# Kernel optimization log

Hardware: AMD Instinct MI355X
Metric: run time of the kernel (lower is better)

## Reference

```python
import jax, jax.numpy as jnp
import numpy as np

D_MODEL = 1024
D_ATTN = 256


def setup_inputs() -> dict:
    key = jax.random.key(0)
    kx, kq, kk, kv = jax.random.split(key, 4)
    B, T = 4, 2048
    s = 1.0 / np.sqrt(D_MODEL)
    return {
        "x": jax.random.normal(kx, (B, T, D_MODEL), dtype=jnp.float32),
        "W_q": jax.random.normal(kq, (D_MODEL, D_ATTN), dtype=jnp.float32) * s,
        "W_k": jax.random.normal(kk, (D_MODEL, D_ATTN), dtype=jnp.float32) * s,
        "W_v": jax.random.normal(kv, (D_MODEL, D_MODEL), dtype=jnp.float32) * s,
    }


def reference(x, W_q, W_k, W_v):
    # x: [B, T, D]; single-head causal self-attention
    B, T, D = x.shape
    scale = jnp.sqrt(jnp.asarray(W_q.shape[-1], dtype=x.dtype))
    Q = jnp.einsum('btd,da->bta', x, W_q)  # [B,T,d_attn]
    K = jnp.einsum('btd,da->bta', x, W_k)  # [B,T,d_attn]
    V = jnp.einsum('btd,de->bte', x, W_v)  # [B,T,d_model]
    scores = jnp.einsum('bqa,bka->bqk', Q, K) / scale  # [B,T,T]
    causal = jnp.tril(jnp.ones((T, T), dtype=bool))
    scores = jnp.where(causal[None], scores, -jnp.inf)
    attn_weights = jax.nn.softmax(scores, axis=-1)
    attn_output = jnp.einsum('bqk,bke->bqe', attn_weights, V)  # [B,T,d_model]
    return (attn_output, attn_weights)
```

## Files before the change

kernel.cpp:

```cpp
#include <hip/hip_runtime.h>


typedef short bf16x8 __attribute__((ext_vector_type(8)));
typedef float f32x4  __attribute__((ext_vector_type(4)));
typedef unsigned int  u32x4 __attribute__((ext_vector_type(4)));
typedef unsigned short u16x4 __attribute__((ext_vector_type(4)));

static __device__ __forceinline__ unsigned short f2bf(float f) {
    union { float f; unsigned int u; } v; v.f = f;
    unsigned int u = v.u;
    return (unsigned short)((u + 0x7FFFu + ((u >> 16) & 1u)) >> 16);
}
static __device__ __forceinline__ float bf2f(unsigned short h) {
    union { unsigned int u; float f; } v; v.u = ((unsigned int)h) << 16; return v.f;
}

#define GLL(g, l) __builtin_amdgcn_global_load_lds( \
    (const __attribute__((address_space(1))) void*)(g), \
    (__attribute__((address_space(3))) void*)(l), 16, 0, 0)

#define BAR() __builtin_amdgcn_s_barrier()
#define VM8() asm volatile("s_waitcnt vmcnt(8)" ::: "memory")
#define VM0() asm volatile("s_waitcnt vmcnt(0)" ::: "memory")


#define STAGE1(AB, LDA, BB, LDB, t, p) { \
    const unsigned short* Ap_ = (AB) + (size_t)(t) * 64; \
    const unsigned short* Bp_ = (BB) + (size_t)(t) * 64; \
    _Pragma("unroll") \
    for (int i_ = 0; i_ < 4; ++i_) { \
        GLL(Ap_ + (size_t)32 * i_ * (LDA), &As[p][srow + 32 * i_][scol]); \
        GLL(Bp_ + (size_t)32 * i_ * (LDB), &Bs[p][srow + 32 * i_][scol]); \
    } }

#define PIPE_MFMA(AB, LDA, BB, LDB, NT) { \
    STAGE1(AB, LDA, BB, LDB, 0, 0); \
    STAGE1(AB, LDA, BB, LDB, 1, 1); \
    for (int t = 0; t < (NT); ++t) { \
        int p = t & 1; \
        if (t + 1 < (NT)) VM8(); else VM0(); \
        BAR(); \
        _Pragma("unroll") \
        for (int ks = 0; ks < 64; ks += 32) { \
            int fo = ks ? (sw0 ^ 32) : sw0; \
            bf16x8 af[4], bfr[4]; \
            _Pragma("unroll") \
            for (int i = 0; i < 4; ++i) af[i]  = *(const bf16x8*)(&As[p][wr + 16 * i + fr][fo]); \
            _Pragma("unroll") \
            for (int j = 0; j < 4; ++j) bfr[j] = *(const bf16x8*)(&Bs[p][wc + 16 * j + fr][fo]); \
            _Pragma("unroll") \
            for (int i = 0; i < 4; ++i) \
            _Pragma("unroll") \
                for (int j = 0; j < 4; ++j) \
                    acc[i][j] = __builtin_amdgcn_mfma_f32_16x16x32_bf16(af[i], bfr[j], acc[i][j], 0, 0, 0); \
        } \
        BAR(); \
        if (t + 2 < (NT)) STAGE1(AB, LDA, BB, LDB, t + 2, p); \
    } }

#define TILE_IDS() \
    int tid = threadIdx.x; \
    int lane = tid & 63, wave = tid >> 6; \
    int wr = (wave >> 1) * 64, wc = (wave & 1) * 64; \
    int fr = lane & 15; \
    int srow = tid >> 3, scol = (tid & 7) * 8; \
    int scolg = (((tid & 7) ^ (srow & 7)) * 8); \
    int sw0 = (((lane >> 4) ^ (fr & 7)) * 8)


__global__ __launch_bounds__(256) void prep(
    const float* __restrict__ x, const float* __restrict__ Wq,
    const float* __restrict__ Wk, const float* __restrict__ Wv,
    unsigned short* __restrict__ x_bf, unsigned short* __restrict__ Wqk_t,
    unsigned short* __restrict__ Wv_t)
{
    int bid = blockIdx.x, tid = threadIdx.x;
    if (bid < 8192) {
        int i = bid * 256 + tid;
        f32x4 v = ((const f32x4*)x)[i];
        u16x4 o;
        o[0] = f2bf(v[0]); o[1] = f2bf(v[1]); o[2] = f2bf(v[2]); o[3] = f2bf(v[3]);
        ((u16x4*)x_bf)[i] = o;
        return;
    }
    const float* W; unsigned short* Wt; int N, lb; float scale;
    if (bid < 8448)      { W = Wq; Wt = Wqk_t;              N = 256;  lb = bid - 8192; scale = 1.f / 16.f; }
    else if (bid < 8704) { W = Wk; Wt = Wqk_t + 256 * 1024; N = 256;  lb = bid - 8448; scale = 1.f; }
    else                 { W = Wv; Wt = Wv_t;               N = 1024; lb = bid - 8704; scale = 1.f; }
    int nb = N >> 5;
    int n0 = (lb % nb) * 32, k0 = (lb / nb) * 32;
    int tx = tid & 31, ty = tid >> 5;
    __shared__ float tile[32][33];
#pragma unroll
    for (int r = 0; r < 4; ++r)
        tile[ty + 8 * r][tx] = W[(size_t)(k0 + ty + 8 * r) * N + n0 + tx];
    __syncthreads();
#pragma unroll
    for (int r = 0; r < 4; ++r)
        Wt[(size_t)(n0 + ty + 8 * r) * 1024 + k0 + tx] = f2bf(tile[tx][ty + 8 * r] * scale);
}


__global__ __launch_bounds__(256) void gemm_qkvt(
    const unsigned short* __restrict__ x_bf,
    const unsigned short* __restrict__ Wqk_t,
    const unsigned short* __restrict__ Wv_t,
    unsigned short* __restrict__ QK_bf,
    unsigned short* __restrict__ Vt_bf)
{
    int bid = blockIdx.x;
    const unsigned short *A, *B; unsigned short* C; int ldc, m0, n0;
    if (bid < 512) {
        A = Wv_t; B = x_bf; C = Vt_bf; ldc = 8192;
        m0 = (bid >> 6) * 128; n0 = (bid & 63) * 128;
    } else {
        int b2 = bid - 512;
        A = x_bf; B = Wqk_t; C = QK_bf; ldc = 512;
        m0 = (b2 >> 2) * 128; n0 = (b2 & 3) * 128;
    }
    __shared__ __align__(16) unsigned short As[2][128][64];
    __shared__ __align__(16) unsigned short Bs[2][128][64];
    TILE_IDS();
    f32x4 acc[4][4] = {};
    const unsigned short* Ab = A + (size_t)(m0 + srow) * 1024 + scolg;
    const unsigned short* Bb = B + (size_t)(n0 + srow) * 1024 + scolg;
    PIPE_MFMA(Ab, 1024, Bb, 1024, 16);
#pragma unroll
    for (int i = 0; i < 4; ++i)
#pragma unroll
        for (int j = 0; j < 4; ++j)
#pragma unroll
            for (int r = 0; r < 4; ++r) {
                int row = m0 + wr + 16 * i + (lane >> 4) * 4 + r;
                int col = n0 + wc + 16 * j + fr;
                C[(size_t)row * ldc + col] = f2bf(acc[i][j][r]);
            }
}


__global__ __launch_bounds__(256) void scores_e(
    const unsigned short* __restrict__ QK, unsigned short* __restrict__ Ebf,
    float* __restrict__ partials)
{
    int lin = blockIdx.x;
    int swz = (lin & 7) * 68 + (lin >> 3);
    int b = swz / 136, t = swz - b * 136;
    int y = (int)floorf((sqrtf(8.f * (float)t + 1.f) - 1.f) * 0.5f);
    if ((y + 1) * (y + 2) / 2 <= t) ++y;
    if (y * (y + 1) / 2 > t) --y;
    int x = t - y * (y + 1) / 2;
    int m0 = y * 128, n0 = x * 128;

    const unsigned short* A  = QK + (size_t)b * 2048 * 512;
    const unsigned short* Bt = A + 256;
    unsigned short* Eb = Ebf + (size_t)b * 2048 * 2048;

    __shared__ __align__(16) unsigned short As[2][128][64];
    __shared__ __align__(16) unsigned short Bs[2][128][64];
    __shared__ float rowsum2[2][128];
    TILE_IDS();
    f32x4 acc[4][4] = {};
    const unsigned short* Ab = A  + (size_t)(m0 + srow) * 512 + scolg;
    const unsigned short* Bb = Bt + (size_t)(n0 + srow) * 512 + scolg;
    PIPE_MFMA(Ab, 512, Bb, 512, 4);

#pragma unroll
    for (int i = 0; i < 4; ++i)
#pragma unroll
        for (int r = 0; r < 4; ++r) {
            int q = m0 + wr + 16 * i + (lane >> 4) * 4 + r;
            float s = 0.f;
#pragma unroll
            for (int j = 0; j < 4; ++j) {
                int k = n0 + wc + 16 * j + fr;
                float e = (k <= q) ? __expf(acc[i][j][r]) : 0.f;
                Eb[(size_t)q * 2048 + k] = f2bf(e);
                s += e;
            }
            s += __shfl_xor(s, 1, 64); s += __shfl_xor(s, 2, 64);
            s += __shfl_xor(s, 4, 64); s += __shfl_xor(s, 8, 64);
            if (fr == 0) rowsum2[wave & 1][wr + 16 * i + (lane >> 4) * 4 + r] = s;
        }
    __syncthreads();
    if (tid < 128)
        partials[((size_t)b * 2048 + m0 + tid) * 16 + x] =
            rowsum2[0][tid] + rowsum2[1][tid];
}


__global__ __launch_bounds__(256) void pv_fin(
    const unsigned short* __restrict__ E, const unsigned short* __restrict__ Vt,
    const float* __restrict__ partials, float* __restrict__ O,
    float* __restrict__ W)
{
    int bid = blockIdx.x;
    __shared__ __align__(16) unsigned short As[2][128][64];
    __shared__ __align__(16) unsigned short Bs[2][128][64];
    __shared__ float invsh[128];

    if (bid < 512) {
        int j   = bid & 7;
        int idx = bid >> 3;
        int x   = idx & 7;
        int h   = idx >> 3;
        int b   = h >> 1;
        int y   = (h & 1) ? j : 15 - j;

        int m0 = y * 128, n0 = x * 128;
        const unsigned short* Pb = E + (size_t)b * 2048 * 2048;
        const unsigned short* Bt = Vt + (size_t)b * 2048;
        float* Ob = O + (size_t)b * 2048 * 1024;
        int nt = (y + 1) * 2;

        TILE_IDS();
        f32x4 acc[4][4] = {};

        if (tid < 128) {
            const float* pp = partials + ((size_t)b * 2048 + m0 + tid) * 16;
            float s = 0.f;
            for (int i = 0; i <= y; ++i) s += pp[i];
            invsh[tid] = 1.f / s;
        }

        const unsigned short* Ab = Pb + (size_t)(m0 + srow) * 2048 + scolg;
        const unsigned short* Bb = Bt + (size_t)(n0 + srow) * 8192 + scolg;
        PIPE_MFMA(Ab, 2048, Bb, 8192, nt);
#pragma unroll
        for (int i = 0; i < 4; ++i)
#pragma unroll
            for (int r = 0; r < 4; ++r) {
                int rloc = wr + 16 * i + (lane >> 4) * 4 + r;
                float iv = invsh[rloc];
#pragma unroll
                for (int jj = 0; jj < 4; ++jj)
                    Ob[(size_t)(m0 + rloc) * 1024 + n0 + wc + 16 * jj + fr] = acc[i][jj][r] * iv;
            }
        return;
    }

    int tid = threadIdx.x;
    int wave = tid >> 6, lane = tid & 63;
    int r = (bid - 512) * 4 + wave;
    int q = r & 2047;
    float p = (lane < 16 && lane <= (q >> 7)) ? partials[(size_t)r * 16 + lane] : 0.f;
    p += __shfl_xor(p, 1, 64); p += __shfl_xor(p, 2, 64);
    p += __shfl_xor(p, 4, 64); p += __shfl_xor(p, 8, 64);
    float iv = 1.f / __shfl(p, 0, 64);
    const unsigned short* er = E + (size_t)r * 2048;
    float* wrow = W + (size_t)r * 2048;
#pragma unroll
    for (int cc = 0; cc < 4; ++cc) {
        int c0 = lane * 8 + cc * 512;
        f32x4 o0 = {}, o1 = {};
        if (c0 <= q) {
            bf16x8 e = *(const bf16x8*)(er + c0);
#pragma unroll
            for (int j = 0; j < 4; ++j) {
                o0[j] = bf2f((unsigned short)e[j]) * iv;
                o1[j] = bf2f((unsigned short)e[j + 4]) * iv;
            }
        }
        *((f32x4*)(wrow + c0)) = o0;
        *((f32x4*)(wrow + c0) + 1) = o1;
    }
}


extern "C" void kernel_launch(void* const* d_in, const int* in_sizes, int n_in,
                              void* d_out, int out_size, void* d_ws, size_t ws_size,
                              hipStream_t stream) {
    (void)in_sizes; (void)n_in; (void)out_size; (void)ws_size;
    const float* x  = (const float*)d_in[0];
    const float* Wq = (const float*)d_in[1];
    const float* Wk = (const float*)d_in[2];
    const float* Wv = (const float*)d_in[3];
    const int B = 4, T = 2048, D = 1024;
    const int M = B * T;

    char* ws = (char*)d_ws;
    size_t off = 0;
    auto alloc = [&](size_t bytes) {
        void* p = ws + off; off += (bytes + 255) & ~(size_t)255; return p;
    };
    unsigned short* x_bf  = (unsigned short*)alloc((size_t)M * D * 2);
    unsigned short* Wqk_t = (unsigned short*)alloc((size_t)512 * D * 2);
    unsigned short* Wv_t  = (unsigned short*)alloc((size_t)D * D * 2);
    unsigned short* QK_bf = (unsigned short*)alloc((size_t)M * 512 * 2);
    unsigned short* Vt_bf = (unsigned short*)alloc((size_t)D * M * 2);
    unsigned short* E_bf  = (unsigned short*)alloc((size_t)M * T * 2);
    float*          parts = (float*)alloc((size_t)M * 16 * 4);

    float* outO = (float*)d_out;
    float* outW = (float*)d_out + (size_t)M * D;

    prep<<<dim3(8192 + 256 + 256 + 1024), 256, 0, stream>>>(
        x, Wq, Wk, Wv, x_bf, Wqk_t, Wv_t);

    gemm_qkvt<<<dim3(768), 256, 0, stream>>>(x_bf, Wqk_t, Wv_t, QK_bf, Vt_bf);

    scores_e<<<dim3(544), 256, 0, stream>>>(QK_bf, E_bf, parts);

    pv_fin<<<dim3(512 + 2048), 256, 0, stream>>>(E_bf, Vt_bf, parts, outO, outW);
}
```

Baseline: 110.1 us.

## Move V projection alongside scores and pre-zero upper-triangle weights in prep

The V^T projection GEMM moves out of the QK projection kernel and into the same launch as the scores kernel, so the 512 V tiles run concurrently with the 544 causal score tiles instead of delaying them. The prep kernel gains 480 extra blocks that write zeros into the fully masked upper-triangle 128x128 tiles of the attention-weight output. The finalize pass then skips those tiles and writes only up to the end of each row's diagonal tile. This spreads the output store traffic across kernels and shortens the critical path, at the cost of a larger heterogeneous scores launch.

```diff
diff --git a/kernel.cpp b/kernel.cpp
--- a/kernel.cpp
+++ b/kernel.cpp
@@ -72,7 +72,7 @@
     const float* __restrict__ x, const float* __restrict__ Wq,
     const float* __restrict__ Wk, const float* __restrict__ Wv,
     unsigned short* __restrict__ x_bf, unsigned short* __restrict__ Wqk_t,
-    unsigned short* __restrict__ Wv_t)
+    unsigned short* __restrict__ Wv_t, float* __restrict__ Wout)
 {
     int bid = blockIdx.x, tid = threadIdx.x;
     if (bid < 8192) {
@@ -83,6 +83,19 @@
         ((u16x4*)x_bf)[i] = o;
         return;
     }
+    if (bid >= 9728) {
+        int t = bid - 9728;
+        int b = t / 120; t -= b * 120;
+        int y = 0, rem = t;
+        while (rem >= 15 - y) { rem -= 15 - y; ++y; }
+        int xx = y + 1 + rem;
+        float* base = Wout + (size_t)b * 2048 * 2048
+                    + (size_t)(y * 128 + (tid >> 1)) * 2048 + xx * 128 + (tid & 1) * 64;
+        f32x4 z = {};
+#pragma unroll
+        for (int i = 0; i < 16; ++i) ((f32x4*)base)[i] = z;
+        return;
+    }
     const float* W; unsigned short* Wt; int N, lb; float scale;
     if (bid < 8448)      { W = Wq; Wt = Wqk_t;              N = 256;  lb = bid - 8192; scale = 1.f / 16.f; }
     else if (bid < 8704) { W = Wk; Wt = Wqk_t + 256 * 1024; N = 256;  lb = bid - 8448; scale = 1.f; }
@@ -101,48 +114,62 @@
 }
 
 
-__global__ __launch_bounds__(256) void gemm_qkvt(
+__global__ __launch_bounds__(256) void gemm_qk(
     const unsigned short* __restrict__ x_bf,
     const unsigned short* __restrict__ Wqk_t,
-    const unsigned short* __restrict__ Wv_t,
-    unsigned short* __restrict__ QK_bf,
-    unsigned short* __restrict__ Vt_bf)
+    unsigned short* __restrict__ QK_bf)
 {
     int bid = blockIdx.x;
-    const unsigned short *A, *B; unsigned short* C; int ldc, m0, n0;
-    if (bid < 512) {
-        A = Wv_t; B = x_bf; C = Vt_bf; ldc = 8192;
-        m0 = (bid >> 6) * 128; n0 = (bid & 63) * 128;
-    } else {
-        int b2 = bid - 512;
-        A = x_bf; B = Wqk_t; C = QK_bf; ldc = 512;
-        m0 = (b2 >> 2) * 128; n0 = (b2 & 3) * 128;
-    }
+    int m0 = (bid >> 2) * 128, n0 = (bid & 3) * 128;
     __shared__ __align__(16) unsigned short As[2][128][64];
     __shared__ __align__(16) unsigned short Bs[2][128][64];
     TILE_IDS();
     f32x4 acc[4][4] = {};
-    const unsigned short* Ab = A + (size_t)(m0 + srow) * 1024 + scolg;
-    const unsigned short* Bb = B + (size_t)(n0 + srow) * 1024 + scolg;
+    const unsigned short* Ab = x_bf + (size_t)(m0 + srow) * 1024 + scolg;
+    const unsigned short* Bb = Wqk_t + (size_t)(n0 + srow) * 1024 + scolg;
     PIPE_MFMA(Ab, 1024, Bb, 1024, 16);
 #pragma unroll
     for (int i = 0; i < 4; ++i)
 #pragma unroll
         for (int j = 0; j < 4; ++j)
 #pragma unroll
-            for (int r = 0; r < 4; ++r) {
-                int row = m0 + wr + 16 * i + (lane >> 4) * 4 + r;
-                int col = n0 + wc + 16 * j + fr;
-                C[(size_t)row * ldc + col] = f2bf(acc[i][j][r]);
-            }
-}
-
-
-__global__ __launch_bounds__(256) void scores_e(
-    const unsigned short* __restrict__ QK, unsigned short* __restrict__ Ebf,
+            for (int r = 0; r < 4; ++r)
+                QK_bf[(size_t)(m0 + wr + 16 * i + (lane >> 4) * 4 + r) * 512
+                      + n0 + wc + 16 * j + fr] = f2bf(acc[i][j][r]);
+}
+
+
+__global__ __launch_bounds__(256) void vt_scores(
+    const unsigned short* __restrict__ x_bf,
+    const unsigned short* __restrict__ Wv_t,
+    const unsigned short* __restrict__ QK,
+    unsigned short* __restrict__ Vt_bf,
+    unsigned short* __restrict__ Ebf,
     float* __restrict__ partials)
 {
-    int lin = blockIdx.x;
+    int bid = blockIdx.x;
+    __shared__ __align__(16) unsigned short As[2][128][64];
+    __shared__ __align__(16) unsigned short Bs[2][128][64];
+
+    if (bid < 512) {
+        int m0 = (bid >> 6) * 128, n0 = (bid & 63) * 128;
+        TILE_IDS();
+        f32x4 acc[4][4] = {};
+        const unsigned short* Ab = Wv_t + (size_t)(m0 + srow) * 1024 + scolg;
+        const unsigned short* Bb = x_bf + (size_t)(n0 + srow) * 1024 + scolg;
+        PIPE_MFMA(Ab, 1024, Bb, 1024, 16);
+#pragma unroll
+        for (int i = 0; i < 4; ++i)
+#pragma unroll
+            for (int j = 0; j < 4; ++j)
+#pragma unroll
+                for (int r = 0; r < 4; ++r)
+                    Vt_bf[(size_t)(m0 + wr + 16 * i + (lane >> 4) * 4 + r) * 8192
+                          + n0 + wc + 16 * j + fr] = f2bf(acc[i][j][r]);
+        return;
+    }
+
+    int lin = bid - 512;
     int swz = (lin & 7) * 68 + (lin >> 3);
     int b = swz / 136, t = swz - b * 136;
     int y = (int)floorf((sqrtf(8.f * (float)t + 1.f) - 1.f) * 0.5f);
@@ -155,8 +182,6 @@
     const unsigned short* Bt = A + 256;
     unsigned short* Eb = Ebf + (size_t)b * 2048 * 2048;
 
-    __shared__ __align__(16) unsigned short As[2][128][64];
-    __shared__ __align__(16) unsigned short Bs[2][128][64];
     __shared__ float rowsum2[2][128];
     TILE_IDS();
     f32x4 acc[4][4] = {};
@@ -242,6 +267,7 @@
     int wave = tid >> 6, lane = tid & 63;
     int r = (bid - 512) * 4 + wave;
     int q = r & 2047;
+    int tile_end = ((q >> 7) + 1) << 7;
     float p = (lane < 16 && lane <= (q >> 7)) ? partials[(size_t)r * 16 + lane] : 0.f;
     p += __shfl_xor(p, 1, 64); p += __shfl_xor(p, 2, 64);
     p += __shfl_xor(p, 4, 64); p += __shfl_xor(p, 8, 64);
@@ -251,6 +277,7 @@
 #pragma unroll
     for (int cc = 0; cc < 4; ++cc) {
         int c0 = lane * 8 + cc * 512;
+        if (c0 >= tile_end) continue;
         f32x4 o0 = {}, o1 = {};
         if (c0 <= q) {
             bf16x8 e = *(const bf16x8*)(er + c0);
@@ -293,12 +320,13 @@
     float* outO = (float*)d_out;
     float* outW = (float*)d_out + (size_t)M * D;
 
-    prep<<<dim3(8192 + 256 + 256 + 1024), 256, 0, stream>>>(
-        x, Wq, Wk, Wv, x_bf, Wqk_t, Wv_t);
-
-    gemm_qkvt<<<dim3(768), 256, 0, stream>>>(x_bf, Wqk_t, Wv_t, QK_bf, Vt_bf);
-
-    scores_e<<<dim3(544), 256, 0, stream>>>(QK_bf, E_bf, parts);
+    prep<<<dim3(8192 + 256 + 256 + 1024 + 480), 256, 0, stream>>>(
+        x, Wq, Wk, Wv, x_bf, Wqk_t, Wv_t, outW);
+
+    gemm_qk<<<dim3(256), 256, 0, stream>>>(x_bf, Wqk_t, QK_bf);
+
+    vt_scores<<<dim3(512 + 544), 256, 0, stream>>>(
+        x_bf, Wv_t, QK_bf, Vt_bf, E_bf, parts);
 
     pv_fin<<<dim3(512 + 2048), 256, 0, stream>>>(E_bf, Vt_bf, parts, outO, outW);
 }
```

Result: slower. 126.8 us (+15.2%).

## Move upper-triangle zero fill to prep and reorder block schedules

Applied to the files above, without the earlier changes.

Zeroing of the fully masked attention-weight tiles above the diagonal moves into the prep kernel as 480 extra blocks, so the finalize pass only writes columns up to the diagonal tile of each row band. The x conversion blocks now each handle four chunks. The QK and V projection GEMM blocks are interleaved in a 1:2 ratio, and the PV and finalize blocks are remapped with a y-band interleave, aiming for better load balance and cache locality across CUs. The cost is a more complex index mapping and more work in the memory-bound prep kernel.

```diff
diff --git a/kernel.cpp b/kernel.cpp
--- a/kernel.cpp
+++ b/kernel.cpp
@@ -67,26 +67,48 @@
     int scolg = (((tid & 7) ^ (srow & 7)) * 8); \
     int sw0 = (((lane >> 4) ^ (fr & 7)) * 8)
 
+static __device__ __forceinline__ int ymem(int G, int yi) {
+    return (yi == 0) ? G : (yi == 1) ? 7 - G : (yi == 2) ? 8 + G : 15 - G;
+}
+
 
 __global__ __launch_bounds__(256) void prep(
     const float* __restrict__ x, const float* __restrict__ Wq,
     const float* __restrict__ Wk, const float* __restrict__ Wv,
     unsigned short* __restrict__ x_bf, unsigned short* __restrict__ Wqk_t,
-    unsigned short* __restrict__ Wv_t)
+    unsigned short* __restrict__ Wv_t, float* __restrict__ Wout)
 {
     int bid = blockIdx.x, tid = threadIdx.x;
-    if (bid < 8192) {
+    if (bid < 2048) {
+        const f32x4* src = (const f32x4*)x;
+        u16x4* dst = (u16x4*)x_bf;
         int i = bid * 256 + tid;
-        f32x4 v = ((const f32x4*)x)[i];
-        u16x4 o;
-        o[0] = f2bf(v[0]); o[1] = f2bf(v[1]); o[2] = f2bf(v[2]); o[3] = f2bf(v[3]);
-        ((u16x4*)x_bf)[i] = o;
+#pragma unroll
+        for (int s = 0; s < 4; ++s) {
+            f32x4 v = src[i + s * 524288];
+            u16x4 o;
+            o[0] = f2bf(v[0]); o[1] = f2bf(v[1]); o[2] = f2bf(v[2]); o[3] = f2bf(v[3]);
+            dst[i + s * 524288] = o;
+        }
         return;
     }
+    if (bid < 2528) {
+        int t = bid - 2048;
+        int b = t / 120; t -= b * 120;
+        int y = 0, rem = t;
+        while (rem >= 15 - y) { rem -= 15 - y; ++y; }
+        int xx = y + 1 + rem;
+        float* base = Wout + (size_t)b * 2048 * 2048
+                    + (size_t)(y * 128 + (tid >> 1)) * 2048 + xx * 128 + (tid & 1) * 64;
+        f32x4 z = {};
+#pragma unroll
+        for (int i = 0; i < 16; ++i) ((f32x4*)base)[i] = z;
+        return;
+    }
     const float* W; unsigned short* Wt; int N, lb; float scale;
-    if (bid < 8448)      { W = Wq; Wt = Wqk_t;              N = 256;  lb = bid - 8192; scale = 1.f / 16.f; }
-    else if (bid < 8704) { W = Wk; Wt = Wqk_t + 256 * 1024; N = 256;  lb = bid - 8448; scale = 1.f; }
-    else                 { W = Wv; Wt = Wv_t;               N = 1024; lb = bid - 8704; scale = 1.f; }
+    if (bid < 2784)      { W = Wq; Wt = Wqk_t;              N = 256;  lb = bid - 2528; scale = 1.f / 16.f; }
+    else if (bid < 3040) { W = Wk; Wt = Wqk_t + 256 * 1024; N = 256;  lb = bid - 2784; scale = 1.f; }
+    else                 { W = Wv; Wt = Wv_t;               N = 1024; lb = bid - 3040; scale = 1.f; }
     int nb = N >> 5;
     int n0 = (lb % nb) * 32, k0 = (lb / nb) * 32;
     int tx = tid & 31, ty = tid >> 5;
@@ -109,14 +131,15 @@
     unsigned short* __restrict__ Vt_bf)
 {
     int bid = blockIdx.x;
+    int g = bid / 3, r3 = bid - 3 * g;
     const unsigned short *A, *B; unsigned short* C; int ldc, m0, n0;
-    if (bid < 512) {
+    if (r3 == 2) {
+        A = x_bf; B = Wqk_t; C = QK_bf; ldc = 512;
+        m0 = (g >> 2) * 128; n0 = (g & 3) * 128;
+    } else {
+        int v = 2 * g + r3;
         A = Wv_t; B = x_bf; C = Vt_bf; ldc = 8192;
-        m0 = (bid >> 6) * 128; n0 = (bid & 63) * 128;
-    } else {
-        int b2 = bid - 512;
-        A = x_bf; B = Wqk_t; C = QK_bf; ldc = 512;
-        m0 = (b2 >> 2) * 128; n0 = (b2 & 3) * 128;
+        m0 = (v >> 6) * 128; n0 = (v & 63) * 128;
     }
     __shared__ __align__(16) unsigned short As[2][128][64];
     __shared__ __align__(16) unsigned short Bs[2][128][64];
@@ -130,11 +153,9 @@
 #pragma unroll
         for (int j = 0; j < 4; ++j)
 #pragma unroll
-            for (int r = 0; r < 4; ++r) {
-                int row = m0 + wr + 16 * i + (lane >> 4) * 4 + r;
-                int col = n0 + wc + 16 * j + fr;
-                C[(size_t)row * ldc + col] = f2bf(acc[i][j][r]);
-            }
+            for (int r = 0; r < 4; ++r)
+                C[(size_t)(m0 + wr + 16 * i + (lane >> 4) * 4 + r) * ldc
+                  + n0 + wc + 16 * j + fr] = f2bf(acc[i][j][r]);
 }
 
 
@@ -199,12 +220,11 @@
     __shared__ float invsh[128];
 
     if (bid < 512) {
-        int j   = bid & 7;
-        int idx = bid >> 3;
-        int x   = idx & 7;
-        int h   = idx >> 3;
-        int b   = h >> 1;
-        int y   = (h & 1) ? j : 15 - j;
+        int j = bid & 7, w = bid >> 3;
+        int G = j >> 1, X = j & 1;
+        int x  = X * 4 + (w >> 4);
+        int y  = ymem(G, (w >> 2) & 3);
+        int b  = w & 3;
 
         int m0 = y * 128, n0 = x * 128;
         const unsigned short* Pb = E + (size_t)b * 2048 * 2048;
@@ -238,11 +258,20 @@
         return;
     }
 
+    int s = bid - 512;
+    int j = s & 7, i = s >> 3;
+    int G = j >> 1, pband = j & 1;
+    int idx2 = i * 2 + pband;
+    int y  = ymem(G, idx2 >> 7);
+    int rb = (idx2 >> 2) & 31;
+    int b  = idx2 & 3;
+
     int tid = threadIdx.x;
     int wave = tid >> 6, lane = tid & 63;
-    int r = (bid - 512) * 4 + wave;
-    int q = r & 2047;
-    float p = (lane < 16 && lane <= (q >> 7)) ? partials[(size_t)r * 16 + lane] : 0.f;
+    int q = y * 128 + rb * 4 + wave;
+    int r = b * 2048 + q;
+    int tile_end = (y + 1) * 128;
+    float p = (lane < 16 && lane <= y) ? partials[(size_t)r * 16 + lane] : 0.f;
     p += __shfl_xor(p, 1, 64); p += __shfl_xor(p, 2, 64);
     p += __shfl_xor(p, 4, 64); p += __shfl_xor(p, 8, 64);
     float iv = 1.f / __shfl(p, 0, 64);
@@ -251,13 +280,14 @@
 #pragma unroll
     for (int cc = 0; cc < 4; ++cc) {
         int c0 = lane * 8 + cc * 512;
+        if (c0 >= tile_end) continue;
         f32x4 o0 = {}, o1 = {};
         if (c0 <= q) {
             bf16x8 e = *(const bf16x8*)(er + c0);
 #pragma unroll
-            for (int j = 0; j < 4; ++j) {
-                o0[j] = bf2f((unsigned short)e[j]) * iv;
-                o1[j] = bf2f((unsigned short)e[j + 4]) * iv;
+            for (int jj = 0; jj < 4; ++jj) {
+                o0[jj] = bf2f((unsigned short)e[jj]) * iv;
+                o1[jj] = bf2f((unsigned short)e[jj + 4]) * iv;
             }
         }
         *((f32x4*)(wrow + c0)) = o0;
@@ -293,8 +323,8 @@
     float* outO = (float*)d_out;
     float* outW = (float*)d_out + (size_t)M * D;
 
-    prep<<<dim3(8192 + 256 + 256 + 1024), 256, 0, stream>>>(
-        x, Wq, Wk, Wv, x_bf, Wqk_t, Wv_t);
+    prep<<<dim3(2048 + 480 + 256 + 256 + 1024), 256, 0, stream>>>(
+        x, Wq, Wk, Wv, x_bf, Wqk_t, Wv_t, outW);
 
     gemm_qkvt<<<dim3(768), 256, 0, stream>>>(x_bf, Wqk_t, Wv_t, QK_bf, Vt_bf);
 
```

Result: slower. 116.4 us (+5.8%).

## Use 256-row PV tiles with 512 threads and triple-buffered loads

Applied to the files above, without the earlier changes.

The PV GEMM moves from 128x128 tiles with 256 threads to 256x128 tiles with 512 threads (8 waves) and a three-stage global-to-LDS pipeline. Each tile now covers two 128-row diagonal blocks, so prep zeroes the strictly-upper diagonal sub-blocks of E that scores_e never writes. The per-row normalization now uses a row-specific limit. The normalize/weights part also runs 8 rows per block. This halves the number of V tile reloads and deepens latency hiding, at the cost of more LDS per block, which may lower occupancy, and some extra MFMA work on the zeroed block.

```diff
diff --git a/kernel.cpp b/kernel.cpp
--- a/kernel.cpp
+++ b/kernel.cpp
@@ -20,8 +20,10 @@
     (__attribute__((address_space(3))) void*)(l), 16, 0, 0)
 
 #define BAR() __builtin_amdgcn_s_barrier()
-#define VM8() asm volatile("s_waitcnt vmcnt(8)" ::: "memory")
-#define VM0() asm volatile("s_waitcnt vmcnt(0)" ::: "memory")
+#define VM12() asm volatile("s_waitcnt vmcnt(12)" ::: "memory")
+#define VM8()  asm volatile("s_waitcnt vmcnt(8)" ::: "memory")
+#define VM6()  asm volatile("s_waitcnt vmcnt(6)" ::: "memory")
+#define VM0()  asm volatile("s_waitcnt vmcnt(0)" ::: "memory")
 
 
 #define STAGE1(AB, LDA, BB, LDB, t, p) { \
@@ -72,7 +74,7 @@
     const float* __restrict__ x, const float* __restrict__ Wq,
     const float* __restrict__ Wk, const float* __restrict__ Wv,
     unsigned short* __restrict__ x_bf, unsigned short* __restrict__ Wqk_t,
-    unsigned short* __restrict__ Wv_t)
+    unsigned short* __restrict__ Wv_t, unsigned short* __restrict__ Ebf)
 {
     int bid = blockIdx.x, tid = threadIdx.x;
     if (bid < 8192) {
@@ -81,6 +83,16 @@
         u16x4 o;
         o[0] = f2bf(v[0]); o[1] = f2bf(v[1]); o[2] = f2bf(v[2]); o[3] = f2bf(v[3]);
         ((u16x4*)x_bf)[i] = o;
+        return;
+    }
+    if (bid >= 9728) {
+        int t = bid - 9728;
+        int b = t >> 3, g = t & 7;
+        unsigned short* base = Ebf + (size_t)b * 2048 * 2048
+            + (size_t)(2 * g * 128 + (tid >> 1)) * 2048 + (2 * g + 1) * 128 + (tid & 1) * 64;
+        u16x4 z = {};
+#pragma unroll
+        for (int i = 0; i < 16; ++i) ((u16x4*)base)[i] = z;
         return;
     }
     const float* W; unsigned short* Wt; int N, lb; float scale;
@@ -130,11 +142,9 @@
 #pragma unroll
         for (int j = 0; j < 4; ++j)
 #pragma unroll
-            for (int r = 0; r < 4; ++r) {
-                int row = m0 + wr + 16 * i + (lane >> 4) * 4 + r;
-                int col = n0 + wc + 16 * j + fr;
-                C[(size_t)row * ldc + col] = f2bf(acc[i][j][r]);
-            }
+            for (int r = 0; r < 4; ++r)
+                C[(size_t)(m0 + wr + 16 * i + (lane >> 4) * 4 + r) * ldc
+                  + n0 + wc + 16 * j + fr] = f2bf(acc[i][j][r]);
 }
 
 
@@ -188,43 +198,78 @@
 }
 
 
-__global__ __launch_bounds__(256) void pv_fin(
+__global__ __launch_bounds__(512) void pv_fin(
     const unsigned short* __restrict__ E, const unsigned short* __restrict__ Vt,
     const float* __restrict__ partials, float* __restrict__ O,
     float* __restrict__ W)
 {
     int bid = blockIdx.x;
-    __shared__ __align__(16) unsigned short As[2][128][64];
-    __shared__ __align__(16) unsigned short Bs[2][128][64];
-    __shared__ float invsh[128];
-
-    if (bid < 512) {
-        int j   = bid & 7;
-        int idx = bid >> 3;
-        int x   = idx & 7;
-        int h   = idx >> 3;
-        int b   = h >> 1;
-        int y   = (h & 1) ? j : 15 - j;
-
-        int m0 = y * 128, n0 = x * 128;
+    __shared__ __align__(16) unsigned short As3[3][256][64];
+    __shared__ __align__(16) unsigned short Bs3[3][128][64];
+    __shared__ float invsh[256];
+
+    if (bid < 256) {
+        int j = bid & 7, w = bid >> 3;
+        int G = j >> 1, X = j & 1;
+        int y = (w & 1) ? 7 - G : G;
+        int x = X * 4 + ((w >> 1) & 3);
+        int b = (w >> 3) & 3;
+
+        int m0 = y * 256, n0 = x * 128;
         const unsigned short* Pb = E + (size_t)b * 2048 * 2048;
         const unsigned short* Bt = Vt + (size_t)b * 2048;
         float* Ob = O + (size_t)b * 2048 * 1024;
-        int nt = (y + 1) * 2;
+        int nt = (y + 1) * 4;
 
         TILE_IDS();
         f32x4 acc[4][4] = {};
 
-        if (tid < 128) {
+        if (tid < 256) {
+            int lim = (m0 + tid) >> 7;
             const float* pp = partials + ((size_t)b * 2048 + m0 + tid) * 16;
             float s = 0.f;
-            for (int i = 0; i <= y; ++i) s += pp[i];
+            for (int i = 0; i <= lim; ++i) s += pp[i];
             invsh[tid] = 1.f / s;
         }
 
         const unsigned short* Ab = Pb + (size_t)(m0 + srow) * 2048 + scolg;
         const unsigned short* Bb = Bt + (size_t)(n0 + srow) * 8192 + scolg;
-        PIPE_MFMA(Ab, 2048, Bb, 8192, nt);
+
+#define PSTAGE(t, p) { \
+        const unsigned short* Ap_ = Ab + (size_t)(t) * 64; \
+        const unsigned short* Bp_ = Bb + (size_t)(t) * 64; \
+        _Pragma("unroll") \
+        for (int i_ = 0; i_ < 4; ++i_) \
+            GLL(Ap_ + (size_t)64 * i_ * 2048, &As3[p][srow + 64 * i_][scol]); \
+        _Pragma("unroll") \
+        for (int i_ = 0; i_ < 2; ++i_) \
+            GLL(Bp_ + (size_t)64 * i_ * 8192, &Bs3[p][srow + 64 * i_][scol]); \
+        }
+
+        PSTAGE(0, 0); PSTAGE(1, 1); PSTAGE(2, 2);
+        int p = 0;
+        for (int t = 0; t < nt; ++t) {
+            int fut = nt - 1 - t; if (fut > 2) fut = 2;
+            if (fut == 2) VM12(); else if (fut == 1) VM6(); else VM0();
+            BAR();
+#pragma unroll
+            for (int ks = 0; ks < 64; ks += 32) {
+                int fo = ks ? (sw0 ^ 32) : sw0;
+                bf16x8 af[4], bfr[4];
+#pragma unroll
+                for (int i = 0; i < 4; ++i) af[i]  = *(const bf16x8*)(&As3[p][wr + 16 * i + fr][fo]);
+#pragma unroll
+                for (int jj = 0; jj < 4; ++jj) bfr[jj] = *(const bf16x8*)(&Bs3[p][wc + 16 * jj + fr][fo]);
+#pragma unroll
+                for (int i = 0; i < 4; ++i)
+#pragma unroll
+                    for (int jj = 0; jj < 4; ++jj)
+                        acc[i][jj] = __builtin_amdgcn_mfma_f32_16x16x32_bf16(af[i], bfr[jj], acc[i][jj], 0, 0, 0);
+            }
+            BAR();
+            if (t + 3 < nt) PSTAGE(t + 3, p);
+            p = (p == 2) ? 0 : p + 1;
+        }
 #pragma unroll
         for (int i = 0; i < 4; ++i)
 #pragma unroll
@@ -240,7 +285,7 @@
 
     int tid = threadIdx.x;
     int wave = tid >> 6, lane = tid & 63;
-    int r = (bid - 512) * 4 + wave;
+    int r = (bid - 256) * 8 + wave;
     int q = r & 2047;
     float p = (lane < 16 && lane <= (q >> 7)) ? partials[(size_t)r * 16 + lane] : 0.f;
     p += __shfl_xor(p, 1, 64); p += __shfl_xor(p, 2, 64);
@@ -255,9 +300,9 @@
         if (c0 <= q) {
             bf16x8 e = *(const bf16x8*)(er + c0);
 #pragma unroll
-            for (int j = 0; j < 4; ++j) {
-                o0[j] = bf2f((unsigned short)e[j]) * iv;
-                o1[j] = bf2f((unsigned short)e[j + 4]) * iv;
+            for (int jj = 0; jj < 4; ++jj) {
+                o0[jj] = bf2f((unsigned short)e[jj]) * iv;
+                o1[jj] = bf2f((unsigned short)e[jj + 4]) * iv;
             }
         }
         *((f32x4*)(wrow + c0)) = o0;
@@ -293,12 +338,12 @@
     float* outO = (float*)d_out;
     float* outW = (float*)d_out + (size_t)M * D;
 
-    prep<<<dim3(8192 + 256 + 256 + 1024), 256, 0, stream>>>(
-        x, Wq, Wk, Wv, x_bf, Wqk_t, Wv_t);
+    prep<<<dim3(8192 + 256 + 256 + 1024 + 32), 256, 0, stream>>>(
+        x, Wq, Wk, Wv, x_bf, Wqk_t, Wv_t, E_bf);
 
     gemm_qkvt<<<dim3(768), 256, 0, stream>>>(x_bf, Wqk_t, Wv_t, QK_bf, Vt_bf);
 
     scores_e<<<dim3(544), 256, 0, stream>>>(QK_bf, E_bf, parts);
 
-    pv_fin<<<dim3(512 + 2048), 256, 0, stream>>>(E_bf, Vt_bf, parts, outO, outW);
-}
+    pv_fin<<<dim3(256 + 1024), 512, 0, stream>>>(E_bf, Vt_bf, parts, outO, outW);
+}
```

New measurement: 127.7 us. 16.0% more time.
